# Optimization experiments

Measured on AMD Instinct MI355X. Metric: run time of the kernel, lower is better.

Reference implementation:

```python
import jax, jax.numpy as jnp
import numpy as np

D_MODEL, D_STATE, EXPAND, D_CONV, HEADDIM = 1024, 128, 2, 4, 64
D_INNER = EXPAND * D_MODEL                      # 2048
NHEADS = D_INNER // HEADDIM                     # 32
NGROUPS = 1
CONV_DIM = D_INNER + 2 * NGROUPS * D_STATE      # 2304
D_IN_PROJ = 2 * D_INNER + 2 * NGROUPS * D_STATE + NHEADS  # 4384
BATCH, SEQ = 2, 4096
EPS = 1e-5


def setup_inputs() -> dict:
    key = jax.random.key(0)
    ks = jax.random.split(key, 6)
    sn = lambda k, shape, sc: jax.random.normal(k, shape, jnp.float32) * sc
    # dt_bias such that softplus(dt_bias) spans [1e-3, 0.1] (mamba2 init)
    dt = jnp.linspace(1e-3, 0.1, NHEADS)
    return {
        "x": sn(ks[0], (BATCH, SEQ, D_MODEL), 1.0),
        "ln_w": jnp.ones((D_MODEL,), jnp.float32),
        "ln_b": jnp.zeros((D_MODEL,), jnp.float32),
        "in_proj_w": sn(ks[1], (D_IN_PROJ, D_MODEL), D_MODEL ** -0.5),
        "conv_w": sn(ks[2], (CONV_DIM, D_CONV), D_CONV ** -0.5),
        "conv_b": jnp.zeros((CONV_DIM,), jnp.float32),
        "dt_bias": jnp.log(jnp.expm1(dt)).astype(jnp.float32),
        "A_log": jnp.log(jnp.arange(1, NHEADS + 1, dtype=jnp.float32)),
        "D": jnp.ones((NHEADS,), jnp.float32),
        "norm_w": jnp.ones((D_INNER,), jnp.float32),
        "out_proj_w": sn(ks[3], (D_MODEL, D_INNER), D_INNER ** -0.5),
    }


def _mamba2(u, in_proj_w, conv_w, conv_b, dt_bias, A_log, Dp, norm_w, out_proj_w):
    b, l, _ = u.shape
    zxbcdt = u @ in_proj_w.T                              # [b,l,4384]
    z, xBC, dt = jnp.split(zxbcdt, [D_INNER, D_INNER + CONV_DIM], axis=-1)
    # causal depthwise conv1d over channels, then SiLU
    xBC = jnp.transpose(xBC, (0, 2, 1))                   # [b,conv_dim,l]
    xBC = jax.lax.conv_general_dilated(
        xBC, conv_w[:, None, :], window_strides=(1,),
        padding=[(D_CONV - 1, 0)], feature_group_count=CONV_DIM,
        dimension_numbers=("NCH", "OIH", "NCH"))
    xBC = jax.nn.silu(jnp.transpose(xBC, (0, 2, 1)) + conv_b)
    x, Bm, Cm = jnp.split(xBC, [D_INNER, D_INNER + NGROUPS * D_STATE], axis=-1)
    dt = jax.nn.softplus(dt + dt_bias)                    # [b,l,h]
    A = -jnp.exp(A_log)                                   # [h]
    xh = x.reshape(b, l, NHEADS, HEADDIM)
    # time-major for the selective scan
    dt_t, x_t = jnp.moveaxis(dt, 1, 0), jnp.moveaxis(xh, 1, 0)
    B_t, C_t = jnp.moveaxis(Bm, 1, 0), jnp.moveaxis(Cm, 1, 0)

    def step(h, inputs):
        dtk, xk, Bk, Ck = inputs                          # [b,h],[b,h,p],[b,n],[b,n]
        decay = jnp.exp(dtk * A)                          # [b,h]
        h = h * decay[:, :, None, None] + (dtk[:, :, None, None] * xk[..., None]) * Bk[:, None, None, :]
        y = jnp.einsum("bhpn,bn->bhp", h, Ck)
        return h, y

    h0 = jnp.zeros((b, NHEADS, HEADDIM, D_STATE), u.dtype)
    _, ys = jax.lax.scan(step, h0, (dt_t, x_t, B_t, C_t))  # ys: [l,b,h,p]
    y = jnp.moveaxis(ys, 0, 1) + Dp[None, None, :, None] * xh
    y = y.reshape(b, l, D_INNER)
    # gated RMSNorm: rmsnorm(y * silu(z)) * norm_w
    y = y * jax.nn.silu(z)
    y = y * jax.lax.rsqrt(jnp.mean(y * y, axis=-1, keepdims=True) + EPS) * norm_w
    return y @ out_proj_w.T


def reference(x, ln_w, ln_b, in_proj_w, conv_w, conv_b, dt_bias, A_log, D, norm_w, out_proj_w):
    mu = jnp.mean(x, -1, keepdims=True)
    var = jnp.mean((x - mu) ** 2, -1, keepdims=True)
    xn = (x - mu) * jax.lax.rsqrt(var + EPS) * ln_w + ln_b
    # dropout is identity at inference
    return x + _mamba2(xn, in_proj_w, conv_w, conv_b, dt_bias, A_log, D, norm_w, out_proj_w)
```

## Files before the change

kernel.cpp:

```cpp
#include <hip/hip_runtime.h>
#include <cstdint>

#define D_MODEL 1024
#define D_INNER 2048
#define NHEADS 32
#define HEADDIM 64
#define D_STATE 128
#define CONV_DIM 2304
#define D_IN_PROJ 4384
#define SEQ 4096
#define NROWS 8192
#define NPROJ_PAD 4480
#define TCH 128
#define NCHUNK 32
#define CR 8

typedef float f32x4 __attribute__((ext_vector_type(4)));
typedef __bf16 bf16x8 __attribute__((ext_vector_type(8)));
typedef unsigned short u16;

__device__ __forceinline__ u16 f2bf(float f) {
  uint32_t u = __builtin_bit_cast(uint32_t, f);
  u += 0x7FFFu + ((u >> 16) & 1u);
  return (u16)(u >> 16);
}
__device__ __forceinline__ float bf2f(u16 h) {
  return __builtin_bit_cast(float, (uint32_t)h << 16);
}
__device__ __forceinline__ float dexp(float a) { return expf(fminf(0.f, a)); }
__device__ __forceinline__ int sw(int v) { return (((v & 7) ^ ((v >> 3) & 7)) << 3); }

typedef __attribute__((address_space(1))) const void gv_t;
typedef __attribute__((address_space(3))) void lv_t;
__device__ __forceinline__ void gload_lds16(const void* g, void* l) {
  __builtin_amdgcn_global_load_lds((gv_t*)g, (lv_t*)l, 16, 0, 0);
}

__global__ __launch_bounds__(256) void cvt_pad(const float* __restrict__ s,
                                               u16* __restrict__ d, int n_src, int n_dst) {
  int i = (blockIdx.x * 256 + threadIdx.x) * 4;
  int stride = gridDim.x * 256 * 4;
  for (; i < n_dst; i += stride) {
    ushort4 o;
    if (i < n_src) {
      float4 v = *(const float4*)&s[i];
      o.x = f2bf(v.x); o.y = f2bf(v.y); o.z = f2bf(v.z); o.w = f2bf(v.w);
    } else {
      o.x = o.y = o.z = o.w = 0;
    }
    *(ushort4*)&d[i] = o;
  }
}

__global__ __launch_bounds__(256) void cvt_w2s(const float* __restrict__ s,
                                               const float* __restrict__ nw,
                                               u16* __restrict__ d, int n) {
  int i = (blockIdx.x * 256 + threadIdx.x) * 4;
  int stride = gridDim.x * 256 * 4;
  for (; i < n; i += stride) {
    float4 v = *(const float4*)&s[i];
    int c = i & (D_INNER - 1);
    ushort4 o;
    o.x = f2bf(v.x * nw[c]);
    o.y = f2bf(v.y * nw[c + 1]);
    o.z = f2bf(v.z * nw[c + 2]);
    o.w = f2bf(v.w * nw[c + 3]);
    *(ushort4*)&d[i] = o;
  }
}

__global__ __launch_bounds__(256) void ln_kernel(const float* __restrict__ x,
                                                 const float* __restrict__ w,
                                                 const float* __restrict__ b,
                                                 u16* __restrict__ out) {
  int row = blockIdx.x, tid = threadIdx.x;
  const float4 v = *(const float4*)&x[(long)row * D_MODEL + tid * 4];
  float s1 = v.x + v.y + v.z + v.w;
  float s2 = v.x * v.x + v.y * v.y + v.z * v.z + v.w * v.w;
#pragma unroll
  for (int m = 32; m >= 1; m >>= 1) {
    s1 += __shfl_xor(s1, m);
    s2 += __shfl_xor(s2, m);
  }
  __shared__ float p1[4], p2[4];
  if ((tid & 63) == 0) { p1[tid >> 6] = s1; p2[tid >> 6] = s2; }
  __syncthreads();
  s1 = p1[0] + p1[1] + p1[2] + p1[3];
  s2 = p2[0] + p2[1] + p2[2] + p2[3];
  float mean = s1 * (1.f / D_MODEL);
  float var = s2 * (1.f / D_MODEL) - mean * mean;
  float rstd = rsqrtf(var + 1e-5f);
  const float4 wv = *(const float4*)&w[tid * 4];
  const float4 bv = *(const float4*)&b[tid * 4];
  ushort4 o;
  o.x = f2bf((v.x - mean) * rstd * wv.x + bv.x);
  o.y = f2bf((v.y - mean) * rstd * wv.y + bv.y);
  o.z = f2bf((v.z - mean) * rstd * wv.z + bv.z);
  o.w = f2bf((v.w - mean) * rstd * wv.w + bv.w);
  *(ushort4*)&out[(long)row * D_MODEL + tid * 4] = o;
}

template <int MODE>
__global__ __launch_bounds__(256, 4) void gemm_bt(const u16* __restrict__ A,
                                                  const u16* __restrict__ B, int K,
                                                  u16* __restrict__ zb,
                                                  u16* __restrict__ xb,
                                                  float* __restrict__ dtb,
                                                  float* __restrict__ C,
                                                  const float* __restrict__ resid,
                                                  const float* __restrict__ rvec) {
  __shared__ __align__(16) u16 As[128 * 64];
  __shared__ __align__(16) u16 Bs[128 * 64];
  const int tid = threadIdx.x;
  int m0, n0;
  if (MODE == 0) {
    const int k = (blockIdx.x & 7) * 280 + (blockIdx.x >> 3);
    const int st = k / 40, inner = k % 40;
    m0 = ((st & 7) * 8 + (inner & 7)) * 128;
    n0 = ((st >> 3) * 5 + (inner >> 3)) * 128;
  } else {
    const int wg = (blockIdx.x & 7) * 64 + (blockIdx.x >> 3);
    m0 = (wg & 63) * 128;
    n0 = (wg >> 6) * 128;
  }
  const int w = tid >> 6, l = tid & 63;
  const int wm = w >> 1, wn = w & 1;

  f32x4 acc[4][4] = {};

  for (int k0 = 0; k0 < K; k0 += 64) {
#pragma unroll
    for (int i = 0; i < 4; ++i) {
      int idx = i * 256 + tid;
      int row = idx >> 3, slot = idx & 7;
      int ks = slot ^ (row & 7);
      const u16* ga = A + (long)(m0 + row) * K + k0 + ks * 8;
      gload_lds16(ga, (char*)As + idx * 16);
      const u16* gb = B + (long)(n0 + row) * K + k0 + ks * 8;
      gload_lds16(gb, (char*)Bs + idx * 16);
    }
    __syncthreads();
    bf16x8 af[2][4], bfr[2][4];
#pragma unroll
    for (int kk = 0; kk < 2; ++kk)
#pragma unroll
      for (int f = 0; f < 4; ++f) {
        int rowa = wm * 64 + f * 16 + (l & 15);
        int ca = ((kk << 2) | (l >> 4)) ^ (rowa & 7);
        af[kk][f] = *(const bf16x8*)((const char*)As + rowa * 128 + ca * 16);
        int rowb = wn * 64 + f * 16 + (l & 15);
        int cb2 = ((kk << 2) | (l >> 4)) ^ (rowb & 7);
        bfr[kk][f] = *(const bf16x8*)((const char*)Bs + rowb * 128 + cb2 * 16);
      }
#pragma unroll
    for (int kk = 0; kk < 2; ++kk)
#pragma unroll
      for (int mf = 0; mf < 4; ++mf)
#pragma unroll
        for (int nf = 0; nf < 4; ++nf)
          acc[mf][nf] = __builtin_amdgcn_mfma_f32_16x16x32_bf16(
              af[kk][mf], bfr[kk][nf], acc[mf][nf], 0, 0, 0);
    __syncthreads();
  }
#pragma unroll
  for (int mf = 0; mf < 4; ++mf)
#pragma unroll
    for (int nf = 0; nf < 4; ++nf) {
      int col = n0 + wn * 64 + nf * 16 + (l & 15);
#pragma unroll
      for (int r = 0; r < 4; ++r) {
        int rowm = m0 + wm * 64 + mf * 16 + (l >> 4) * 4 + r;
        float v = acc[mf][nf][r];
        if (MODE == 0) {
          if (col < D_INNER)
            zb[(long)rowm * D_INNER + col] = f2bf(v);
          else if (col < D_INNER + CONV_DIM)
            xb[(long)rowm * CONV_DIM + (col - D_INNER)] = f2bf(v);
          else if (col < D_IN_PROJ)
            dtb[(long)rowm * NHEADS + (col - D_INNER - CONV_DIM)] = v;
        } else {
          long off = (long)rowm * D_MODEL + col;
          C[off] = v * rvec[rowm] + resid[off];
        }
      }
    }
}

__global__ __launch_bounds__(256) void conv_silu_kernel(const u16* __restrict__ xr,
                                                        const float* __restrict__ cw,
                                                        const float* __restrict__ cb,
                                                        u16* __restrict__ xp,
                                                        u16* __restrict__ bc) {
  const int c = blockIdx.x * 256 + threadIdx.x;
  const int row0 = blockIdx.y * CR;
  const int t0 = row0 & (SEQ - 1);
  const float4 wv = *(const float4*)&cw[c * 4];
  const float bias = cb[c];
  float xwin[CR + 3];
#pragma unroll
  for (int k = 0; k < CR + 3; ++k) {
    int t = t0 - 3 + k;
    xwin[k] = (t >= 0) ? bf2f(xr[(long)(row0 - 3 + k) * CONV_DIM + c]) : 0.f;
  }
#pragma unroll
  for (int j = 0; j < CR; ++j) {
    float a = bias + xwin[j] * wv.x + xwin[j + 1] * wv.y + xwin[j + 2] * wv.z +
              xwin[j + 3] * wv.w;
    a = a / (1.f + expf(-a));
    int row = row0 + j;
    if (c < D_INNER)
      xp[(long)row * D_INNER + c] = f2bf(a);
    else
      bc[(long)row * (2 * D_STATE) + (c - D_INNER)] = f2bf(a);
  }
}

__global__ __launch_bounds__(64) void dt_pre(const float* __restrict__ dtf,
                                             const float* __restrict__ dt_bias,
                                             const float* __restrict__ A_log,
                                             float* __restrict__ sgb,
                                             float* __restrict__ dsb,
                                             float* __restrict__ egb) {
  const int cc = blockIdx.x, hh = blockIdx.y, bb = blockIdx.z;
  const int l = threadIdx.x;
  const float Ah = -expf(A_log[hh]);
  const float dbias = dt_bias[hh];
  const long rowbase = (long)bb * SEQ + cc * TCH;
  float r0 = dtf[(rowbase + l) * NHEADS + hh] + dbias;
  float r1 = dtf[(rowbase + 64 + l) * NHEADS + hh] + dbias;
  float d0 = r0 > 20.f ? r0 : log1pf(expf(r0));
  float d1 = r1 > 20.f ? r1 : log1pf(expf(r1));
  float a0 = d0 * Ah, a1 = d1 * Ah;
#pragma unroll
  for (int d = 1; d < 64; d <<= 1) { float u = __shfl_up(a0, d); if (l >= d) a0 += u; }
#pragma unroll
  for (int d = 1; d < 64; d <<= 1) { float u = __shfl_up(a1, d); if (l >= d) a1 += u; }
  float t0 = __shfl(a0, 63);
  float s1 = a1 + t0;
  const long idx = ((long)(bb * 32 + hh) * 32 + cc) * 128;
  sgb[idx + l] = a0;       sgb[idx + 64 + l] = s1;
  dsb[idx + l] = d0;       dsb[idx + 64 + l] = d1;
  egb[idx + l] = dexp(a0); egb[idx + 64 + l] = dexp(s1);
}

__global__ __launch_bounds__(256, 2) void ssd_g_kernel(const u16* __restrict__ bcb,
                                                       u16* __restrict__ Gsw) {
  const int cc = blockIdx.x, bb = blockIdx.y;
  const int tid = threadIdx.x, w = tid >> 6, l = tid & 63;
  const long rowbase = (long)bb * SEQ + cc * TCH;
  bf16x8 cfr[2][4];
#pragma unroll
  for (int tt = 0; tt < 2; ++tt) {
    int t = (w * 2 + tt) * 16 + (l & 15);
#pragma unroll
    for (int kc = 0; kc < 4; ++kc)
      cfr[tt][kc] = *(const bf16x8*)&bcb[(rowbase + t) * 256 + 128 + kc * 32 +
                                         (l >> 4) * 8];
  }
  f32x4 g[2][8] = {};
#pragma unroll
  for (int st = 0; st < 8; ++st) {
    int s = st * 16 + (l & 15);
#pragma unroll
    for (int kc = 0; kc < 4; ++kc) {
      bf16x8 bfv = *(const bf16x8*)&bcb[(rowbase + s) * 256 + kc * 32 + (l >> 4) * 8];
      g[0][st] = __builtin_amdgcn_mfma_f32_16x16x32_bf16(cfr[0][kc], bfv, g[0][st], 0, 0, 0);
      g[1][st] = __builtin_amdgcn_mfma_f32_16x16x32_bf16(cfr[1][kc], bfv, g[1][st], 0, 0, 0);
    }
  }
  u16* Gb = Gsw + (long)(bb * 32 + cc) * 16384;
#pragma unroll
  for (int tt = 0; tt < 2; ++tt)
#pragma unroll
    for (int st = 0; st < 8; ++st)
#pragma unroll
      for (int r = 0; r < 4; ++r) {
        int t = (w * 2 + tt) * 16 + (l >> 4) * 4 + r;
        int s = st * 16 + (l & 15);
        int j = ((((s >> 3) ^ (t & 15)) << 3) | (s & 7));
        Gb[t * 128 + j] = f2bf(g[tt][st][r]);
      }
}

__global__ __launch_bounds__(256, 3) void ssd_state_kernel(
    const u16* __restrict__ xp, const u16* __restrict__ bcb,
    const float* __restrict__ dtf, const float* __restrict__ dt_bias,
    const float* __restrict__ A_log, u16* __restrict__ S,
    float* __restrict__ cdk) {
  const int hh = blockIdx.x, cc = blockIdx.y, bb = blockIdx.z;
  const int tid = threadIdx.x, w = tid >> 6, l = tid & 63;
  __shared__ __align__(16) u16 BT[128 * 128];
  __shared__ __align__(16) u16 WXT[64 * 128];
  __shared__ float ws[128];
  const long rowbase = (long)bb * SEQ + cc * TCH;
  const float Ah = -expf(A_log[hh]);
  const float dbias = dt_bias[hh];

#pragma unroll
  for (int i = 0; i < 8; ++i) {
    int slot = i * 256 + tid, t = slot >> 4, nb = slot & 15;
    bf16x8 v = *(const bf16x8*)&bcb[(rowbase + t) * 256 + nb * 8];
    const u16* e = (const u16*)&v;
#pragma unroll
    for (int j = 0; j < 8; ++j) {
      int n = nb * 8 + j;
      BT[n * 128 + (t ^ sw(n))] = e[j];
    }
  }
  if (w == 0) {
    float r0 = dtf[(rowbase + l) * NHEADS + hh] + dbias;
    float r1 = dtf[(rowbase + 64 + l) * NHEADS + hh] + dbias;
    float d0 = r0 > 20.f ? r0 : log1pf(expf(r0));
    float d1 = r1 > 20.f ? r1 : log1pf(expf(r1));
    float a0 = d0 * Ah, a1 = d1 * Ah;
#pragma unroll
    for (int d = 1; d < 64; d <<= 1) { float u = __shfl_up(a0, d); if (l >= d) a0 += u; }
#pragma unroll
    for (int d = 1; d < 64; d <<= 1) { float u = __shfl_up(a1, d); if (l >= d) a1 += u; }
    float t0 = __shfl(a0, 63);
    float tot = __shfl(a1, 63) + t0;
    ws[l] = dexp(tot - a0) * d0;
    ws[64 + l] = dexp(tot - (a1 + t0)) * d1;
    if (l == 0) cdk[(bb * 32 + hh) * NCHUNK + cc] = dexp(tot);
  }
  __syncthreads();
#pragma unroll
  for (int i = 0; i < 4; ++i) {
    int slot = i * 256 + tid, t = slot >> 3, pb = slot & 7;
    bf16x8 v = *(const bf16x8*)&xp[(rowbase + t) * D_INNER + hh * 64 + pb * 8];
    float wt = ws[t];
    const u16* e = (const u16*)&v;
#pragma unroll
    for (int j = 0; j < 8; ++j) {
      int p = pb * 8 + j;
      WXT[p * 128 + (t ^ sw(p))] = f2bf(bf2f(e[j]) * wt);
    }
  }
  __syncthreads();

  f32x4 acc[8] = {};
  const int p = w * 16 + (l & 15);
  const int swp = sw(p);
#pragma unroll
  for (int kc = 0; kc < 4; ++kc) {
    int tsl = kc * 32 + (l >> 4) * 8;
    bf16x8 af = *(const bf16x8*)&WXT[p * 128 + (tsl ^ swp)];
#pragma unroll
    for (int nt = 0; nt < 8; ++nt) {
      int n = nt * 16 + (l & 15);
      bf16x8 bfv = *(const bf16x8*)&BT[n * 128 + (tsl ^ sw(n))];
      acc[nt] = __builtin_amdgcn_mfma_f32_16x16x32_bf16(af, bfv, acc[nt], 0, 0, 0);
    }
  }
  u16* Sb = S + ((long)(bb * 32 + hh) * NCHUNK + cc) * 8192;
#pragma unroll
  for (int nt = 0; nt < 8; ++nt)
#pragma unroll
    for (int r = 0; r < 4; ++r) {
      int prow = w * 16 + (l >> 4) * 4 + r;
      Sb[prow * 128 + nt * 16 + (l & 15)] = f2bf(acc[nt][r]);
    }
}

__global__ __launch_bounds__(256) void ssd_combine(u16* __restrict__ SH,
                                                   const float* __restrict__ cdk) {
  const int hh = blockIdx.y, bb = blockIdx.z;
  const int pp = blockIdx.x * 16 + (threadIdx.x >> 4);
  const int nn = (threadIdx.x & 15) * 8;
  const int bh = bb * 32 + hh;
  u16* base = SH + (long)bh * NCHUNK * 8192 + pp * 128 + nn;
  const float* ck = cdk + bh * NCHUNK;
  float h[8] = {};
  for (int c = 0; c < NCHUNK; ++c) {
    bf16x8 sv = *(bf16x8*)(base + (long)c * 8192);
    const u16* se = (const u16*)&sv;
    u16 o[8];
#pragma unroll
    for (int j = 0; j < 8; ++j) o[j] = f2bf(h[j]);
    *(bf16x8*)(base + (long)c * 8192) = *(bf16x8*)o;
    float d = ck[c];
#pragma unroll
    for (int j = 0; j < 8; ++j) h[j] = fmaf(h[j], d, bf2f(se[j]));
  }
}

__global__ __launch_bounds__(256, 3) void ssd_y_kernel(
    const u16* __restrict__ xp, const u16* __restrict__ bcb,
    const u16* __restrict__ Gsw, const float* __restrict__ sgb,
    const float* __restrict__ dsb, const float* __restrict__ egb,
    const float* __restrict__ Dp, const u16* __restrict__ H,
    u16* __restrict__ zb, float* __restrict__ psum) {
  const int hh = blockIdx.x, cc = blockIdx.y, bb = blockIdx.z;
  const int tid = threadIdx.x, w = tid >> 6, l = tid & 63;
  __shared__ __align__(16) u16 Gs[128 * 128];
  __shared__ __align__(16) u16 XT[64 * 128];
  __shared__ float sig[128], dts[128], esg[128];
  const long rowbase = (long)bb * SEQ + cc * TCH;
  const float Dh = Dp[hh];

  const u16* Gb = Gsw + (long)(bb * 32 + cc) * 16384;
#pragma unroll
  for (int i = 0; i < 8; ++i) {
    int idx = i * 256 + tid;
    gload_lds16(Gb + idx * 8, (char*)Gs + idx * 16);
  }
  const long sidx = ((long)(bb * 32 + hh) * 32 + cc) * 128;
  if (tid < 128) {
    sig[tid] = sgb[sidx + tid];
    dts[tid] = dsb[sidx + tid];
    esg[tid] = egb[sidx + tid];
  }
#pragma unroll
  for (int i = 0; i < 4; ++i) {
    int slot = i * 256 + tid, t = slot >> 3, pb = slot & 7;
    bf16x8 v = *(const bf16x8*)&xp[(rowbase + t) * D_INNER + hh * 64 + pb * 8];
    const u16* e = (const u16*)&v;
#pragma unroll
    for (int j = 0; j < 8; ++j) {
      int p = pb * 8 + j;
      XT[p * 128 + (t ^ sw(p))] = e[j];
    }
  }
  bf16x8 cfr[2][4];
#pragma unroll
  for (int tt = 0; tt < 2; ++tt) {
    int t = (w * 2 + tt) * 16 + (l & 15);
#pragma unroll
    for (int kc = 0; kc < 4; ++kc)
      cfr[tt][kc] = *(const bf16x8*)&bcb[(rowbase + t) * 256 + 128 + kc * 32 +
                                         (l >> 4) * 8];
  }
  __syncthreads();

  {
    const int t = tid >> 1, half = tid & 1;
    const float sigt = sig[t];
#pragma unroll
    for (int wb = 0; wb < 8; ++wb) {
      int sblkL = half * 8 + wb;
      int sb2 = sblkL ^ (t & 15);
      bf16x8 v = *(const bf16x8*)&Gs[t * 128 + sb2 * 8];
      const u16* ge = (const u16*)&v;
      u16 o[8];
#pragma unroll
      for (int j = 0; j < 8; ++j) {
        int s = sblkL * 8 + j;
        float m = 0.f;
        if (s <= t) m = bf2f(ge[j]) * dexp(sigt - sig[s]) * dts[s];
        o[j] = f2bf(m);
      }
      *(bf16x8*)&Gs[t * 128 + sb2 * 8] = *(bf16x8*)o;
    }
  }
  __syncthreads();

  f32x4 y1[2][4] = {};
#pragma unroll
  for (int kc = 0; kc < 4; ++kc) {
#pragma unroll
    for (int tt = 0; tt < 2; ++tt) {
      int t = (w * 2 + tt) * 16 + (l & 15);
      int want = kc * 4 + (l >> 4);
      int sb2 = want ^ (t & 15);
      bf16x8 mf = *(const bf16x8*)&Gs[t * 128 + sb2 * 8];
#pragma unroll
      for (int pt = 0; pt < 4; ++pt) {
        int p = pt * 16 + (l & 15);
        int ssl = kc * 32 + (l >> 4) * 8;
        bf16x8 xf = *(const bf16x8*)&XT[p * 128 + (ssl ^ sw(p))];
        y1[tt][pt] = __builtin_amdgcn_mfma_f32_16x16x32_bf16(mf, xf, y1[tt][pt], 0, 0, 0);
      }
    }
  }
  f32x4 y2[2][4] = {};
  const u16* Hb = H + ((long)(bb * 32 + hh) * NCHUNK + cc) * 8192;
#pragma unroll
  for (int pt = 0; pt < 4; ++pt) {
    int p = pt * 16 + (l & 15);
#pragma unroll
    for (int kc = 0; kc < 4; ++kc) {
      bf16x8 hf = *(const bf16x8*)&Hb[p * 128 + kc * 32 + (l >> 4) * 8];
      y2[0][pt] = __builtin_amdgcn_mfma_f32_16x16x32_bf16(cfr[0][kc], hf, y2[0][pt], 0, 0, 0);
      y2[1][pt] = __builtin_amdgcn_mfma_f32_16x16x32_bf16(cfr[1][kc], hf, y2[1][pt], 0, 0, 0);
    }
  }
  float s2[2][4] = {};
#pragma unroll
  for (int tt = 0; tt < 2; ++tt)
#pragma unroll
    for (int pt = 0; pt < 4; ++pt)
#pragma unroll
      for (int r = 0; r < 4; ++r) {
        int t = (w * 2 + tt) * 16 + (l >> 4) * 4 + r;
        int p = pt * 16 + (l & 15);
        float xv = bf2f(XT[p * 128 + (t ^ sw(p))]);
        float yv = y1[tt][pt][r] + esg[t] * y2[tt][pt][r] + Dh * xv;
        long off = (rowbase + t) * (long)D_INNER + hh * 64 + p;
        float zv = bf2f(zb[off]);
        float gg = yv * (zv / (1.f + expf(-zv)));
        zb[off] = f2bf(gg);
        s2[tt][r] += gg * gg;
      }
#pragma unroll
  for (int tt = 0; tt < 2; ++tt)
#pragma unroll
    for (int r = 0; r < 4; ++r) {
      float v = s2[tt][r];
      v += __shfl_xor(v, 1);
      v += __shfl_xor(v, 2);
      v += __shfl_xor(v, 4);
      v += __shfl_xor(v, 8);
      if ((l & 15) == 0) {
        int t = (w * 2 + tt) * 16 + (l >> 4) * 4 + r;
        psum[(rowbase + t) * NHEADS + hh] = v;
      }
    }
}

__global__ __launch_bounds__(256) void r_reduce(const float* __restrict__ psum,
                                                float* __restrict__ rvec) {
  int row = blockIdx.x * 256 + threadIdx.x;
  const float4* p = (const float4*)&psum[(long)row * NHEADS];
  float s = 0.f;
#pragma unroll
  for (int i = 0; i < 8; ++i) {
    float4 v = p[i];
    s += v.x + v.y + v.z + v.w;
  }
  rvec[row] = rsqrtf(s * (1.f / D_INNER) + 1e-5f);
}

extern "C" void kernel_launch(void* const* d_in, const int* in_sizes, int n_in,
                              void* d_out, int out_size, void* d_ws, size_t ws_size,
                              hipStream_t stream) {
  const float* x = (const float*)d_in[0];
  const float* ln_w = (const float*)d_in[1];
  const float* ln_b = (const float*)d_in[2];
  const float* in_proj_w = (const float*)d_in[3];
  const float* conv_w = (const float*)d_in[4];
  const float* conv_b = (const float*)d_in[5];
  const float* dt_bias = (const float*)d_in[6];
  const float* A_log = (const float*)d_in[7];
  const float* Dvec = (const float*)d_in[8];
  const float* norm_w = (const float*)d_in[9];
  const float* out_proj_w = (const float*)d_in[10];
  float* out = (float*)d_out;

  char* ws = (char*)d_ws;
  u16* W2bf = (u16*)(ws + 0);
  u16* zbf = (u16*)(ws + 4194304);
  u16* xpart = (u16*)(ws + 37748736);
  u16* bcbf = (u16*)(ws + 71303168);
  float* dtf = (float*)(ws + 75497472);
  float* cdk = (float*)(ws + 76546048);
  u16* W1bf = (u16*)(ws + 76554240);
  u16* xbcraw = (u16*)(ws + 85729280);
  u16* SH = (u16*)(ws + 76554240);
  float* psum = (float*)(ws + 110108672);
  float* rvec = (float*)(ws + 111157248);
  u16* Gsw = (u16*)(ws + 111190016);
  float* sgb = (float*)(ws + 113287168);
  float* dsb = (float*)(ws + 114335744);
  float* egb = (float*)(ws + 115384320);
  u16* xnbf = (u16*)d_out;

  cvt_pad<<<512, 256, 0, stream>>>(in_proj_w, W1bf, D_IN_PROJ * D_MODEL,
                                   NPROJ_PAD * D_MODEL);
  cvt_w2s<<<512, 256, 0, stream>>>(out_proj_w, norm_w, W2bf, D_MODEL * D_INNER);
  ln_kernel<<<NROWS, 256, 0, stream>>>(x, ln_w, ln_b, xnbf);
  gemm_bt<0><<<35 * 64, 256, 0, stream>>>(xnbf, W1bf, D_MODEL, zbf, xbcraw, dtf,
                                          nullptr, nullptr, nullptr);
  conv_silu_kernel<<<dim3(9, NROWS / CR), 256, 0, stream>>>(xbcraw, conv_w, conv_b,
                                                            xpart, bcbf);
  dt_pre<<<dim3(NCHUNK, NHEADS, 2), 64, 0, stream>>>(dtf, dt_bias, A_log, sgb, dsb,
                                                     egb);
  ssd_g_kernel<<<dim3(NCHUNK, 2), 256, 0, stream>>>(bcbf, Gsw);
  ssd_state_kernel<<<dim3(32, NCHUNK, 2), 256, 0, stream>>>(xpart, bcbf, dtf, dt_bias,
                                                            A_log, SH, cdk);
  ssd_combine<<<dim3(4, 32, 2), 256, 0, stream>>>(SH, cdk);
  ssd_y_kernel<<<dim3(32, NCHUNK, 2), 256, 0, stream>>>(xpart, bcbf, Gsw, sgb, dsb,
                                                        egb, Dvec, SH, zbf, psum);
  r_reduce<<<32, 256, 0, stream>>>(psum, rvec);
  gemm_bt<1><<<8 * 64, 256, 0, stream>>>(zbf, W2bf, D_INNER, nullptr, nullptr,
                                         nullptr, out, x, rvec);
}
```

Before: 285.0 us.

## Precompute swizzled B transpose once per chunk and vectorize gated epilogue via LDS

The B-matrix transpose and swizzle moves out of ssd_state_kernel, which ran it once per head, into ssd_g_kernel, which runs it once per chunk and writes the result to a workspace buffer. ssd_state_kernel then copies that buffer into LDS with direct global-to-LDS loads instead of doing scattered 16-bit LDS stores. Separately, the ssd_y epilogue stages y through LDS so each thread can do 16-byte vectorized z loads and stores and reduce the row sum of squares with a single shuffle. The trade-off is extra workspace traffic, an extra barrier, and a larger LDS footprint in ssd_g_kernel.

New measurement: 285.4 us. About the same (+0.1%).

```diff
diff --git a/kernel.cpp b/kernel.cpp
--- a/kernel.cpp
+++ b/kernel.cpp
@@ -244,10 +244,24 @@
 }
 
 __global__ __launch_bounds__(256, 2) void ssd_g_kernel(const u16* __restrict__ bcb,
-                                                       u16* __restrict__ Gsw) {
+                                                       u16* __restrict__ Gsw,
+                                                       u16* __restrict__ BTsw) {
   const int cc = blockIdx.x, bb = blockIdx.y;
   const int tid = threadIdx.x, w = tid >> 6, l = tid & 63;
+  __shared__ __align__(16) u16 BTl[128 * 128];
   const long rowbase = (long)bb * SEQ + cc * TCH;
+
+#pragma unroll
+  for (int i = 0; i < 8; ++i) {
+    int slot = i * 256 + tid, t = slot >> 4, nb = slot & 15;
+    bf16x8 v = *(const bf16x8*)&bcb[(rowbase + t) * 256 + nb * 8];
+    const u16* e = (const u16*)&v;
+#pragma unroll
+    for (int j = 0; j < 8; ++j) {
+      int n = nb * 8 + j;
+      BTl[n * 128 + (t ^ sw(n))] = e[j];
+    }
+  }
   bf16x8 cfr[2][4];
 #pragma unroll
   for (int tt = 0; tt < 2; ++tt) {
@@ -280,10 +294,17 @@
         int j = ((((s >> 3) ^ (t & 15)) << 3) | (s & 7));
         Gb[t * 128 + j] = f2bf(g[tt][st][r]);
       }
+  __syncthreads();
+  u16* BTo = BTsw + (long)(bb * 32 + cc) * 16384;
+#pragma unroll
+  for (int i = 0; i < 8; ++i) {
+    int idx = i * 256 + tid;
+    *(bf16x8*)&BTo[idx * 8] = *(const bf16x8*)&BTl[idx * 8];
+  }
 }
 
 __global__ __launch_bounds__(256, 3) void ssd_state_kernel(
-    const u16* __restrict__ xp, const u16* __restrict__ bcb,
+    const u16* __restrict__ xp, const u16* __restrict__ BTsw,
     const float* __restrict__ dtf, const float* __restrict__ dt_bias,
     const float* __restrict__ A_log, u16* __restrict__ S,
     float* __restrict__ cdk) {
@@ -296,16 +317,11 @@
   const float Ah = -expf(A_log[hh]);
   const float dbias = dt_bias[hh];
 
+  const u16* BTg = BTsw + (long)(bb * 32 + cc) * 16384;
 #pragma unroll
   for (int i = 0; i < 8; ++i) {
-    int slot = i * 256 + tid, t = slot >> 4, nb = slot & 15;
-    bf16x8 v = *(const bf16x8*)&bcb[(rowbase + t) * 256 + nb * 8];
-    const u16* e = (const u16*)&v;
-#pragma unroll
-    for (int j = 0; j < 8; ++j) {
-      int n = nb * 8 + j;
-      BT[n * 128 + (t ^ sw(n))] = e[j];
-    }
+    int idx = i * 256 + tid;
+    gload_lds16(BTg + idx * 8, (char*)BT + idx * 16);
   }
   if (w == 0) {
     float r0 = dtf[(rowbase + l) * NHEADS + hh] + dbias;
@@ -484,7 +500,7 @@
       y2[1][pt] = __builtin_amdgcn_mfma_f32_16x16x32_bf16(cfr[1][kc], hf, y2[1][pt], 0, 0, 0);
     }
   }
-  float s2[2][4] = {};
+  __syncthreads();
 #pragma unroll
   for (int tt = 0; tt < 2; ++tt)
 #pragma unroll
@@ -495,26 +511,36 @@
         int p = pt * 16 + (l & 15);
         float xv = bf2f(XT[p * 128 + (t ^ sw(p))]);
         float yv = y1[tt][pt][r] + esg[t] * y2[tt][pt][r] + Dh * xv;
-        long off = (rowbase + t) * (long)D_INNER + hh * 64 + p;
-        float zv = bf2f(zb[off]);
+        int blk = (p >> 3) ^ (t & 15);
+        Gs[t * 128 + blk * 8 + (p & 7)] = f2bf(yv);
+      }
+  __syncthreads();
+  {
+    const int t = tid >> 1, half = tid & 1;
+    const long off = (rowbase + t) * (long)D_INNER + hh * 64 + half * 32;
+    float s2 = 0.f;
+#pragma unroll
+    for (int g2 = 0; g2 < 4; ++g2) {
+      int pblk = half * 4 + g2;
+      int lblk = pblk ^ (t & 15);
+      bf16x8 yv8 = *(const bf16x8*)&Gs[t * 128 + lblk * 8];
+      const u16* ye = (const u16*)&yv8;
+      bf16x8 zv8 = *(const bf16x8*)&zb[off + g2 * 8];
+      const u16* ze = (const u16*)&zv8;
+      u16 o[8];
+#pragma unroll
+      for (int j = 0; j < 8; ++j) {
+        float yv = bf2f(ye[j]);
+        float zv = bf2f(ze[j]);
         float gg = yv * (zv / (1.f + expf(-zv)));
-        zb[off] = f2bf(gg);
-        s2[tt][r] += gg * gg;
+        o[j] = f2bf(gg);
+        s2 += gg * gg;
       }
-#pragma unroll
-  for (int tt = 0; tt < 2; ++tt)
-#pragma unroll
-    for (int r = 0; r < 4; ++r) {
-      float v = s2[tt][r];
-      v += __shfl_xor(v, 1);
-      v += __shfl_xor(v, 2);
-      v += __shfl_xor(v, 4);
-      v += __shfl_xor(v, 8);
-      if ((l & 15) == 0) {
-        int t = (w * 2 + tt) * 16 + (l >> 4) * 4 + r;
-        psum[(rowbase + t) * NHEADS + hh] = v;
-      }
-    }
+      *(bf16x8*)&zb[off + g2 * 8] = *(bf16x8*)o;
+    }
+    s2 += __shfl_xor(s2, 1);
+    if (half == 0) psum[(rowbase + t) * NHEADS + hh] = s2;
+  }
 }
 
 __global__ __launch_bounds__(256) void r_reduce(const float* __restrict__ psum,
@@ -562,6 +588,7 @@
   float* sgb = (float*)(ws + 113287168);
   float* dsb = (float*)(ws + 114335744);
   float* egb = (float*)(ws + 115384320);
+  u16* BTsw = (u16*)(ws + 116432896);
   u16* xnbf = (u16*)d_out;
 
   cvt_pad<<<512, 256, 0, stream>>>(in_proj_w, W1bf, D_IN_PROJ * D_MODEL,
@@ -574,8 +601,8 @@
                                                             xpart, bcbf);
   dt_pre<<<dim3(NCHUNK, NHEADS, 2), 64, 0, stream>>>(dtf, dt_bias, A_log, sgb, dsb,
                                                      egb);
-  ssd_g_kernel<<<dim3(NCHUNK, 2), 256, 0, stream>>>(bcbf, Gsw);
-  ssd_state_kernel<<<dim3(32, NCHUNK, 2), 256, 0, stream>>>(xpart, bcbf, dtf, dt_bias,
+  ssd_g_kernel<<<dim3(NCHUNK, 2), 256, 0, stream>>>(bcbf, Gsw, BTsw);
+  ssd_state_kernel<<<dim3(32, NCHUNK, 2), 256, 0, stream>>>(xpart, BTsw, dtf, dt_bias,
                                                             A_log, SH, cdk);
   ssd_combine<<<dim3(4, 32, 2), 256, 0, stream>>>(SH, cdk);
   ssd_y_kernel<<<dim3(32, NCHUNK, 2), 256, 0, stream>>>(xpart, bcbf, Gsw, sgb, dsb,
```
